# Performance work log

Measured on AMD Instinct MI355X. Metric: run time of the kernel, lower is better.

The kernel has to match this reference:

```python
import jax, jax.numpy as jnp
import numpy as np

EPS = 1e-8

def setup_inputs() -> dict:
    key = jax.random.key(0)
    k1, k2, k3, k4 = jax.random.split(key, 4)
    N, D = 65536, 384
    x_candidates = jax.random.normal(k1, (N, D), dtype=jnp.float32)
    y = jax.random.normal(k2, (D,), dtype=jnp.float32)
    z = jax.random.normal(k3, (D,), dtype=jnp.float32)
    a = jax.random.normal(k4, (D, D, D), dtype=jnp.float32)
    return {"x_candidates": x_candidates, "y": y, "z": z, "a": a}

def reference(x_candidates, y, z, a):
    # feature_fn is identity: fy = y, fz = z, fx = each candidate row.
    fy, fz = y, z
    # context[i] = sum_{j,k} a[i,j,k] * fy[j] * fz[k]  (the triple loop, fused)
    # computed as two matvecs to avoid materializing a*fy*fz outer products:
    # tmp[i,j] = sum_k a[i,j,k] * fz[k]; context[i] = sum_j tmp[i,j] * fy[j]
    context = jnp.einsum("ij,j->i", jnp.einsum("ijk,k->ij", a, fz), fy)  # [D]
    # denominator = sum_{j,k} a[0,j,k]*fy[j]*fz[k] == context[0]
    denominator = context[0]
    # score(x) = sum_i fx[i] * context[i] / (denominator + eps)
    scores = (x_candidates @ context) / (denominator + EPS)  # [N]
    return scores
```

## Files before the change

### kernel.cpp

```cpp
#include <hip/hip_runtime.h>

typedef float f32x4 __attribute__((ext_vector_type(4)));

#define EPS 1e-8f

constexpr int D = 384;
constexpr int Q_PER_I = (D * D) / 4;
constexpr int P = 4;
constexpr int Q_PER_PART = Q_PER_I / P;
constexpr int THREADS_A = 256;
constexpr int ITERS_A = Q_PER_PART / THREADS_A;
constexpr int J_PER_PART = 96;

__global__ __launch_bounds__(THREADS_A) void ctx_partial_kernel(
    const float* __restrict__ a,
    const float* __restrict__ y,
    const float* __restrict__ z,
    float* __restrict__ partials) {
  const int b = blockIdx.x;
  const int i = b >> 2;
  const int part = b & 3;
  const f32x4* a4 = reinterpret_cast<const f32x4*>(a) +
                    (size_t)i * Q_PER_I + (size_t)part * Q_PER_PART;
  const f32x4* z4 = reinterpret_cast<const f32x4*>(z);
  const int tid = threadIdx.x;
  const float* yb = y + part * J_PER_PART;

  int jl = tid / 96;
  const int k4 = tid - jl * 96;
  int k4b = k4 + 64; if (k4b >= 96) k4b -= 96;
  int k4c = k4b + 64; if (k4c >= 96) k4c -= 96;
  const f32x4 zva = z4[k4];
  const f32x4 zvb = z4[k4b];
  const f32x4 zvc = z4[k4c];
  const int incA = (k4 >= 32) ? 3 : 2;
  const int incAB = incA + ((k4b >= 32) ? 3 : 2);

  const f32x4* ap = a4 + tid;
  float acc = 0.0f;
#pragma unroll 4
  for (int g = 0; g < ITERS_A / 3; ++g) {
    f32x4 av0 = ap[0 * THREADS_A];
    f32x4 av1 = ap[1 * THREADS_A];
    f32x4 av2 = ap[2 * THREADS_A];
    float ya = yb[jl];
    float yB = yb[jl + incA];
    float yC = yb[jl + incAB];
    acc += ya * (av0.x * zva.x + av0.y * zva.y + av0.z * zva.z + av0.w * zva.w);
    acc += yB * (av1.x * zvb.x + av1.y * zvb.y + av1.z * zvb.z + av1.w * zvb.w);
    acc += yC * (av2.x * zvc.x + av2.y * zvc.y + av2.z * zvc.z + av2.w * zvc.w);
    ap += 3 * THREADS_A;
    jl += 8;
  }

  for (int off = 32; off > 0; off >>= 1)
    acc += __shfl_down(acc, off);

  __shared__ float sm[THREADS_A / 64];
  const int lane = tid & 63;
  const int w = tid >> 6;
  if (lane == 0) sm[w] = acc;
  __syncthreads();
  if (tid == 0) {
    float s = 0.0f;
#pragma unroll
    for (int k = 0; k < THREADS_A / 64; ++k) s += sm[k];
    partials[b] = s;
  }
}

__global__ __launch_bounds__(256) void score_kernel(
    const float* __restrict__ x,
    const float* __restrict__ partials,
    float* __restrict__ out,
    int N) {
  __shared__ float ctx_s[D];
  const int tid = threadIdx.x;

  const f32x4* p4 = reinterpret_cast<const f32x4*>(partials);
  for (int t = tid; t < D; t += 256) {
    f32x4 v = p4[t];
    ctx_s[t] = v.x + v.y + v.z + v.w;
  }
  __syncthreads();

  const float scale = 1.0f / (ctx_s[0] + EPS);
  const int lane = tid & 63;
  const int w = tid >> 6;
  const f32x4* c4 = reinterpret_cast<const f32x4*>(ctx_s);
  const f32x4 cv = c4[lane];
  f32x4 cv2 = {0.f, 0.f, 0.f, 0.f};
  if (lane < 32) cv2 = c4[64 + lane];

  const f32x4* x4 = reinterpret_cast<const f32x4*>(x);
  const int waveId = blockIdx.x * 4 + w;
  const int totalWaves = gridDim.x * 4;
  for (int row = waveId; row < N; row += totalWaves) {
    const f32x4* xr = x4 + (size_t)row * (D / 4);
    f32x4 xv = xr[lane];
    float s = xv.x * cv.x + xv.y * cv.y + xv.z * cv.z + xv.w * cv.w;
    if (lane < 32) {
      f32x4 xv2 = xr[64 + lane];
      s += xv2.x * cv2.x + xv2.y * cv2.y + xv2.z * cv2.z + xv2.w * cv2.w;
    }
    for (int off = 32; off > 0; off >>= 1)
      s += __shfl_down(s, off);
    if (lane == 0) out[row] = s * scale;
  }
}

extern "C" void kernel_launch(void* const* d_in, const int* in_sizes, int n_in,
                              void* d_out, int out_size, void* d_ws, size_t ws_size,
                              hipStream_t stream) {
  const float* x = (const float*)d_in[0];
  const float* y = (const float*)d_in[1];
  const float* z = (const float*)d_in[2];
  const float* a = (const float*)d_in[3];
  float* out = (float*)d_out;

  const int N = in_sizes[0] / D;
  float* partials = (float*)d_ws;

  ctx_partial_kernel<<<D * P, THREADS_A, 0, stream>>>(a, y, z, partials);
  score_kernel<<<2048, 256, 0, stream>>>(x, partials, out, N);
}
```

Baseline: 60.31 us.

## Split context reduction into eight parts and stream inputs with nontemporal loads

```diff
diff --git a/kernel.cpp b/kernel.cpp
--- a/kernel.cpp
+++ b/kernel.cpp
@@ -6,11 +6,15 @@
 
 constexpr int D = 384;
 constexpr int Q_PER_I = (D * D) / 4;
-constexpr int P = 4;
+constexpr int P = 8;
 constexpr int Q_PER_PART = Q_PER_I / P;
 constexpr int THREADS_A = 256;
 constexpr int ITERS_A = Q_PER_PART / THREADS_A;
-constexpr int J_PER_PART = 96;
+constexpr int J_PER_PART = D / P;
+
+__device__ __forceinline__ f32x4 ldnt(const f32x4* p) {
+  return __builtin_nontemporal_load(p);
+}
 
 __global__ __launch_bounds__(THREADS_A) void ctx_partial_kernel(
     const float* __restrict__ a,
@@ -18,8 +22,8 @@
     const float* __restrict__ z,
     float* __restrict__ partials) {
   const int b = blockIdx.x;
-  const int i = b >> 2;
-  const int part = b & 3;
+  const int i = b >> 3;
+  const int part = b & 7;
   const f32x4* a4 = reinterpret_cast<const f32x4*>(a) +
                     (size_t)i * Q_PER_I + (size_t)part * Q_PER_PART;
   const f32x4* z4 = reinterpret_cast<const f32x4*>(z);
@@ -38,11 +42,11 @@
 
   const f32x4* ap = a4 + tid;
   float acc = 0.0f;
-#pragma unroll 4
+#pragma unroll
   for (int g = 0; g < ITERS_A / 3; ++g) {
-    f32x4 av0 = ap[0 * THREADS_A];
-    f32x4 av1 = ap[1 * THREADS_A];
-    f32x4 av2 = ap[2 * THREADS_A];
+    f32x4 av0 = ldnt(ap + 0 * THREADS_A);
+    f32x4 av1 = ldnt(ap + 1 * THREADS_A);
+    f32x4 av2 = ldnt(ap + 2 * THREADS_A);
     float ya = yb[jl];
     float yB = yb[jl + incA];
     float yC = yb[jl + incAB];
@@ -79,8 +83,9 @@
 
   const f32x4* p4 = reinterpret_cast<const f32x4*>(partials);
   for (int t = tid; t < D; t += 256) {
-    f32x4 v = p4[t];
-    ctx_s[t] = v.x + v.y + v.z + v.w;
+    f32x4 v0 = p4[t * 2 + 0];
+    f32x4 v1 = p4[t * 2 + 1];
+    ctx_s[t] = (v0.x + v0.y + v0.z + v0.w) + (v1.x + v1.y + v1.z + v1.w);
   }
   __syncthreads();
 
@@ -95,16 +100,47 @@
   const f32x4* x4 = reinterpret_cast<const f32x4*>(x);
   const int waveId = blockIdx.x * 4 + w;
   const int totalWaves = gridDim.x * 4;
-  for (int row = waveId; row < N; row += totalWaves) {
-    const f32x4* xr = x4 + (size_t)row * (D / 4);
-    f32x4 xv = xr[lane];
-    float s = xv.x * cv.x + xv.y * cv.y + xv.z * cv.z + xv.w * cv.w;
+
+  int row = waveId;
+  while (row + totalWaves < N) {
+    const int r0 = row;
+    const int r1 = row + totalWaves;
+    const f32x4* xr0 = x4 + (size_t)r0 * 96;
+    const f32x4* xr1 = x4 + (size_t)r1 * 96;
+    f32x4 xa0 = ldnt(xr0 + lane);
+    f32x4 xa1 = ldnt(xr1 + lane);
+    f32x4 xb0 = {0.f, 0.f, 0.f, 0.f}, xb1 = {0.f, 0.f, 0.f, 0.f};
     if (lane < 32) {
-      f32x4 xv2 = xr[64 + lane];
-      s += xv2.x * cv2.x + xv2.y * cv2.y + xv2.z * cv2.z + xv2.w * cv2.w;
+      xb0 = ldnt(xr0 + 64 + lane);
+      xb1 = ldnt(xr1 + 64 + lane);
     }
-    for (int off = 32; off > 0; off >>= 1)
-      s += __shfl_down(s, off);
+    float s0 = xa0.x * cv.x + xa0.y * cv.y + xa0.z * cv.z + xa0.w * cv.w;
+    float s1 = xa1.x * cv.x + xa1.y * cv.y + xa1.z * cv.z + xa1.w * cv.w;
+    if (lane < 32) {
+      s0 += xb0.x * cv2.x + xb0.y * cv2.y + xb0.z * cv2.z + xb0.w * cv2.w;
+      s1 += xb1.x * cv2.x + xb1.y * cv2.y + xb1.z * cv2.z + xb1.w * cv2.w;
+    }
+#pragma unroll
+    for (int off = 32; off > 0; off >>= 1) {
+      s0 += __shfl_down(s0, off);
+      s1 += __shfl_down(s1, off);
+    }
+    if (lane == 0) {
+      out[r0] = s0 * scale;
+      out[r1] = s1 * scale;
+    }
+    row += 2 * totalWaves;
+  }
+  if (row < N) {
+    const f32x4* xr = x4 + (size_t)row * 96;
+    f32x4 xa = ldnt(xr + lane);
+    float s = xa.x * cv.x + xa.y * cv.y + xa.z * cv.z + xa.w * cv.w;
+    if (lane < 32) {
+      f32x4 xb = ldnt(xr + 64 + lane);
+      s += xb.x * cv2.x + xb.y * cv2.y + xb.z * cv2.z + xb.w * cv2.w;
+    }
+#pragma unroll
+    for (int off = 32; off > 0; off >>= 1) s += __shfl_down(s, off);
     if (lane == 0) out[row] = s * scale;
   }
 }
```

Measured after the change: 55.83 us. 1.08x faster.
